# Kernel optimization log

Hardware: AMD Instinct MI355X
Metric: run time of the kernel (lower is better)

Reference implementation:

```python
import jax, jax.numpy as jnp
import numpy as np

N_HEAD, D_HEAD, D_MODEL = 16, 64, 1024
BSZ, QLEN, MEMLEN = 4, 1024, 1024
KLEN = QLEN + MEMLEN
LN_EPS = 1e-5


def _rel_shift(x):
    # x: [b, q, k, n] -> Transformer-XL relative shift
    b, q, k, n = x.shape
    x = jnp.pad(x, ((0, 0), (0, 0), (1, 0), (0, 0)))  # [b, q, k+1, n]
    x = x.reshape(b, k + 1, q, n)[:, 1:]
    return x.reshape(b, q, k, n)


def _layer_norm(x, gamma, beta):
    mu = jnp.mean(x, axis=-1, keepdims=True)
    var = jnp.var(x, axis=-1, keepdims=True)
    return (x - mu) * jax.lax.rsqrt(var + LN_EPS) * gamma + beta


def setup_inputs() -> dict:
    key = jax.random.key(0)
    ks = jax.random.split(key, 8)
    w = jax.random.normal(ks[0], (BSZ, QLEN, D_MODEL), dtype=jnp.float32)
    r = jax.random.normal(ks[1], (1, KLEN, D_MODEL), dtype=jnp.float32)
    mem = jax.random.normal(ks[2], (BSZ, MEMLEN, D_MODEL), dtype=jnp.float32)
    # causal mask: key j visible iff j <= i + MEMLEN; 1 = masked
    i = jnp.arange(QLEN)[:, None]
    j = jnp.arange(KLEN)[None, :]
    attention_mask = (j > i + MEMLEN).astype(jnp.int32)
    s = 0.02
    qkv_w = jax.random.normal(ks[3], (3 * N_HEAD * D_HEAD, D_MODEL), dtype=jnp.float32) * s
    r_w = jax.random.normal(ks[4], (N_HEAD * D_HEAD, D_MODEL), dtype=jnp.float32) * s
    o_w = jax.random.normal(ks[5], (D_MODEL, N_HEAD * D_HEAD), dtype=jnp.float32) * s
    r_r_bias = jax.random.normal(ks[6], (N_HEAD, D_HEAD), dtype=jnp.float32) * s
    r_w_bias = jax.random.normal(ks[7], (N_HEAD, D_HEAD), dtype=jnp.float32) * s
    ln_gamma = jnp.ones((D_MODEL,), dtype=jnp.float32)
    ln_beta = jnp.zeros((D_MODEL,), dtype=jnp.float32)
    return {"w": w, "r": r, "mem": mem, "attention_mask": attention_mask,
            "qkv_w": qkv_w, "r_w": r_w, "o_w": o_w,
            "r_r_bias": r_r_bias, "r_w_bias": r_w_bias,
            "ln_gamma": ln_gamma, "ln_beta": ln_beta}


def reference(w, r, mem, attention_mask, qkv_w, r_w, o_w, r_r_bias, r_w_bias, ln_gamma, ln_beta):
    bsz, qlen, d_model = w.shape
    n_head, d_head = r_r_bias.shape
    scale = 1.0 / (d_head ** 0.5)
    cat = jnp.concatenate([mem, w], axis=1)                 # [b, klen, dm]
    heads = cat @ qkv_w.T                                   # post-lnorm: no pre-LN
    q, k, v = jnp.split(heads, 3, axis=-1)
    q = q[:, -qlen:]
    klen = k.shape[1]
    q = q.reshape(bsz, qlen, n_head, d_head)
    k = k.reshape(bsz, klen, n_head, d_head)
    v = v.reshape(bsz, klen, n_head, d_head)
    rk = (r @ r_w.T).reshape(-1, n_head, d_head)            # [rlen, n, d]
    AC = jnp.einsum('bind,bjnd->bijn', q + r_w_bias, k)
    BD = _rel_shift(jnp.einsum('bind,jnd->bijn', q + r_r_bias, rk))
    score = (AC + BD) * scale                               # [b, q, k, n]
    mask = (attention_mask == 1)[None, :, :, None]
    score = jnp.where(mask, -1e30, score)
    prob = jax.nn.softmax(score, axis=2)                    # softmax over keys
    vec = jnp.einsum('bijn,bjnd->bind', prob, v).reshape(bsz, qlen, n_head * d_head)
    attn_out = vec @ o_w.T
    # post layer-norm, deepnorm_alpha defaults to 1.0, dropout is identity (eval)
    return _layer_norm(w + attn_out, ln_gamma, ln_beta)
```

## Files before the change

### kernel.cpp

```cpp
#include <hip/hip_runtime.h>

typedef __attribute__((ext_vector_type(8))) __bf16 bf16x8;
typedef __attribute__((ext_vector_type(4))) __bf16 bf16x4;
typedef __attribute__((ext_vector_type(4))) float f32x4;

#define SCALE_LOG2E 0.18033688011112042f

__device__ __forceinline__ f32x4 mfma16(bf16x8 a, bf16x8 b, f32x4 c) {
  return __builtin_amdgcn_mfma_f32_16x16x32_bf16(a, b, c, 0, 0, 0);
}

__device__ __forceinline__ void gload_lds16(const void* g, void* l) {
  __builtin_amdgcn_global_load_lds(
      (__attribute__((address_space(1))) void*)(void*)g,
      (__attribute__((address_space(3))) void*)l, 16, 0, 0);
}

__device__ __forceinline__ bf16x8 ldsfrag(const __bf16* base, int row, int lc) {
  return *(const bf16x8*)(base + row * 64 + ((lc ^ (row & 7)) << 3));
}


__global__ __launch_bounds__(256) void cast_plain(const float* __restrict__ in,
                                                  __bf16* __restrict__ out) {
  size_t t = (size_t)blockIdx.x * 256 + threadIdx.x;
  const float4* p = (const float4*)(in + t * 8);
  float4 a = p[0], b = p[1];
  bf16x8 v;
  v[0] = (__bf16)a.x; v[1] = (__bf16)a.y; v[2] = (__bf16)a.z; v[3] = (__bf16)a.w;
  v[4] = (__bf16)b.x; v[5] = (__bf16)b.y; v[6] = (__bf16)b.z; v[7] = (__bf16)b.w;
  *(bf16x8*)(out + t * 8) = v;
}

__global__ __launch_bounds__(256) void cast_cat(const float* __restrict__ mem,
                                                const float* __restrict__ w,
                                                __bf16* __restrict__ out) {
  size_t t = (size_t)blockIdx.x * 256 + threadIdx.x;
  size_t o = t * 8;
  int c = (int)(o & 1023);
  int row = (int)(o >> 10);
  int tt = row & 2047;
  int b = row >> 11;
  const float* src = (tt < 1024)
      ? (mem + ((size_t)(b * 1024 + tt) * 1024 + c))
      : (w + ((size_t)(b * 1024 + (tt - 1024)) * 1024 + c));
  float4 a = ((const float4*)src)[0], d = ((const float4*)src)[1];
  bf16x8 v;
  v[0] = (__bf16)a.x; v[1] = (__bf16)a.y; v[2] = (__bf16)a.z; v[3] = (__bf16)a.w;
  v[4] = (__bf16)d.x; v[5] = (__bf16)d.y; v[6] = (__bf16)d.z; v[7] = (__bf16)d.w;
  *(bf16x8*)(out + o) = v;
}

template <int MODE>
__global__ __launch_bounds__(256, 2) void gemm_bt(const __bf16* __restrict__ A,
                                                  const __bf16* __restrict__ B,
                                                  __bf16* __restrict__ Cb,
                                                  float* __restrict__ Cf,
                                                  const float* __restrict__ Res,
                                                  int M, int N, int K, int skipq) {
  if (skipq && blockIdx.x < 8 && (blockIdx.y & 15) < 8) return;
  __shared__ __bf16 As[128 * 32];
  __shared__ __bf16 Bs[128 * 32];
  const int tid = threadIdx.x;
  const int wid = tid >> 6, lane = tid & 63;
  const int l15 = lane & 15, lhi = lane >> 4;
  const int wr = wid >> 1, wc = wid & 1;
  const size_t arow0 = (size_t)blockIdx.y * 128;
  const size_t brow0 = (size_t)blockIdx.x * 128;

  f32x4 acc[4][4] = {};

  const int c0 = tid, c1 = tid + 256;
  const int r0 = c0 >> 2, o0 = (c0 & 3) * 8;
  const int r1 = c1 >> 2, o1 = (c1 & 3) * 8;
  const __bf16* ga0 = A + (arow0 + r0) * K + o0;
  const __bf16* ga1 = A + (arow0 + r1) * K + o1;
  const __bf16* gb0 = B + (brow0 + r0) * K + o0;
  const __bf16* gb1 = B + (brow0 + r1) * K + o1;
  __bf16* la0 = As + wid * 512;
  __bf16* la1 = As + 2048 + wid * 512;
  __bf16* lb0 = Bs + wid * 512;
  __bf16* lb1 = Bs + 2048 + wid * 512;

  for (int k0 = 0; k0 < K; k0 += 32) {
    gload_lds16(ga0 + k0, la0);
    gload_lds16(ga1 + k0, la1);
    gload_lds16(gb0 + k0, lb0);
    gload_lds16(gb1 + k0, lb1);
    __syncthreads();
    bf16x8 af[4], bf[4];
#pragma unroll
    for (int m = 0; m < 4; ++m)
      af[m] = *(const bf16x8*)(As + (wr * 64 + m * 16 + l15) * 32 + lhi * 8);
#pragma unroll
    for (int n = 0; n < 4; ++n)
      bf[n] = *(const bf16x8*)(Bs + (wc * 64 + n * 16 + l15) * 32 + lhi * 8);
#pragma unroll
    for (int m = 0; m < 4; ++m)
#pragma unroll
      for (int n = 0; n < 4; ++n)
        acc[m][n] = mfma16(af[m], bf[n], acc[m][n]);
    __syncthreads();
  }

#pragma unroll
  for (int m = 0; m < 4; ++m)
#pragma unroll
    for (int n = 0; n < 4; ++n) {
      size_t row = arow0 + wr * 64 + m * 16 + lhi * 4;
      size_t col = brow0 + wc * 64 + n * 16 + l15;
#pragma unroll
      for (int j = 0; j < 4; ++j) {
        size_t idx = (row + j) * (size_t)N + col;
        float v = acc[m][n][j];
        if (MODE == 0) Cb[idx] = (__bf16)v;
        else Cf[idx] = v + Res[idx];
      }
    }
}

__global__ __launch_bounds__(256) void vtrans_kernel(const __bf16* __restrict__ heads,
                                                     __bf16* __restrict__ vT) {
  __shared__ __bf16 T[64][66];
  const int j0 = blockIdx.x * 64;
  const int h = blockIdx.y, b = blockIdx.z;
  const int tid = threadIdx.x;
  {
    int jj = tid >> 2, dq = tid & 3;
    const __bf16* src = heads + ((size_t)(b * 2048 + j0 + jj)) * 3072 + 2048 + h * 64 + dq * 16;
    bf16x8 a = *(const bf16x8*)src;
    bf16x8 c = *(const bf16x8*)(src + 8);
#pragma unroll
    for (int e = 0; e < 8; ++e) { T[jj][dq * 16 + e] = a[e]; T[jj][dq * 16 + 8 + e] = c[e]; }
  }
  __syncthreads();
  {
    int d = tid >> 2, jq = tid & 3;
    bf16x8 o0, o1;
#pragma unroll
    for (int e = 0; e < 8; ++e) { o0[e] = T[jq * 16 + e][d]; o1[e] = T[jq * 16 + 8 + e][d]; }
    __bf16* dst = vT + ((size_t)((b * 16 + h) * 64 + d)) * 2048 + j0 + jq * 16;
    *(bf16x8*)dst = o0;
    *(bf16x8*)(dst + 8) = o1;
  }
}

__global__ __launch_bounds__(256) void ackb_kernel(const __bf16* __restrict__ heads,
                                                   const float* __restrict__ r_w_bias,
                                                   float* __restrict__ ackb) {
  int gid = blockIdx.x * 256 + threadIdx.x;
  int j = gid & 2047, bh = gid >> 11, b = bh >> 4, h = bh & 15;
  const __bf16* kp = heads + ((size_t)(b * 2048 + j)) * 3072 + 1024 + h * 64;
  const float* bw = r_w_bias + h * 64;
  float s = 0.f;
#pragma unroll
  for (int o = 0; o < 8; ++o) {
    bf16x8 kv = *(const bf16x8*)(kp + o * 8);
#pragma unroll
    for (int e = 0; e < 8; ++e) s += (float)kv[e] * bw[o * 8 + e];
  }
  ackb[(size_t)bh * 2048 + j] = s * SCALE_LOG2E;
}

__global__ __launch_bounds__(256) void brk_kernel(const __bf16* __restrict__ rk,
                                                  const float* __restrict__ r_r_bias,
                                                  float* __restrict__ brk) {
  int gid = blockIdx.x * 256 + threadIdx.x;
  int t = gid % 2304, h = gid / 2304;
  float s = 0.f;
  if (t < 2048) {
    const __bf16* rp = rk + (size_t)t * 1024 + h * 64;
    const float* br = r_r_bias + h * 64;
#pragma unroll
    for (int o = 0; o < 8; ++o) {
      bf16x8 rv = *(const bf16x8*)(rp + o * 8);
#pragma unroll
      for (int e = 0; e < 8; ++e) s += (float)rv[e] * br[o * 8 + e];
    }
  }
  brk[(size_t)h * 2304 + t] = s * SCALE_LOG2E;
}

__global__ __launch_bounds__(256) void attn_kernel(
    const __bf16* __restrict__ heads, const __bf16* __restrict__ rk,
    const __bf16* __restrict__ vT, const float* __restrict__ ackb,
    const float* __restrict__ brk, __bf16* __restrict__ vec) {
  __shared__ __bf16 Ks[2 * 4096];
  __shared__ __bf16 Vt[2 * 4096];
  __shared__ __bf16 Pool[4][2112];

  const int lin = blockIdx.x;
  const int seq = lin >> 3;
  const int bq = 15 - (seq >> 3);
  const int rem = seq & 7;
  const int b = rem >> 1;
  const int h = (lin & 7) + ((rem & 1) << 3);
  const int base = bq << 6;

  const int tid = threadIdx.x;
  const int wid = tid >> 6, lane = tid & 63;
  const int l15 = lane & 15, lhi = lane >> 4;
  const int i0 = base + wid * 16;

  const int srow8 = lane >> 3;
  const int sch = (lane & 7) ^ (srow8 & 7);

  bf16x8 q0, q1;
  {
    const __bf16* qp =
        heads + ((size_t)(b * 2048 + 1024 + i0 + l15)) * 3072 + h * 64 + lhi * 8;
    bf16x8 a = *(const bf16x8*)qp;
    bf16x8 c = *(const bf16x8*)(qp + 32);
#pragma unroll
    for (int e = 0; e < 8; ++e) {
      q0[e] = (__bf16)((float)a[e] * SCALE_LOG2E);
      q1[e] = (__bf16)((float)c[e] * SCALE_LOG2E);
    }
  }

  const float* ackbp = ackb + ((size_t)(b * 16 + h)) * 2048;
  const float* brkp = brk + (size_t)h * 2304;
  __bf16* BPW = Pool[wid];

  float m_run = -1e30f, l_run = 0.f;
  f32x4 accv[4] = {};

#define STAGE_KV(J0, BUF)                                                              \
  do {                                                                                 \
    const __bf16* kst = heads +                                                        \
        ((size_t)(b * 2048 + (J0) + wid * 16 + srow8)) * 3072 + 1024 + h * 64 + sch * 8; \
    gload_lds16(kst, Ks + (BUF) * 4096 + wid * 16 * 64);                               \
    gload_lds16(kst + (size_t)8 * 3072, Ks + (BUF) * 4096 + (wid * 16 + 8) * 64);      \
    const __bf16* vst = vT +                                                           \
        ((size_t)((b * 16 + h) * 64 + wid * 16 + srow8)) * 2048 + (J0) + sch * 8;      \
    gload_lds16(vst, Vt + (BUF) * 4096 + wid * 16 * 64);                               \
    gload_lds16(vst + (size_t)8 * 2048, Vt + (BUF) * 4096 + (wid * 16 + 8) * 64);      \
  } while (0)

  bf16x8 rka[5][2];
  STAGE_KV(0, 0);
  {
    const int tb0 = 1008 - i0;
#pragma unroll
    for (int ct = 0; ct < 5; ++ct) {
      int t = min(tb0 + ct * 16 + l15, 2047);
      const __bf16* rp = rk + (size_t)t * 1024 + h * 64 + lhi * 8;
      rka[ct][0] = *(const bf16x8*)rp;
      rka[ct][1] = *(const bf16x8*)(rp + 32);
    }
  }

  const int jmaxb = min(2048, base + 1088);
  for (int j0 = 0; j0 < jmaxb; j0 += 64) {
    const int buf = (j0 >> 6) & 1;
    __syncthreads();
    if (j0 + 64 < jmaxb) STAGE_KV(j0 + 64, buf ^ 1);
    if (j0 >= i0 + 1040) continue;

    const __bf16* KsC = Ks + buf * 4096;
    const __bf16* VtC = Vt + buf * 4096;
    const int tbase = j0 + 1008 - i0;

#pragma unroll
    for (int ct = 0; ct < 5; ++ct) {
      int cb = ct * 16 + lhi * 4;
      f32x4 init = *(const f32x4*)(brkp + tbase + cb);
      f32x4 bd = mfma16(rka[ct][1], q1, mfma16(rka[ct][0], q0, init));
      bf16x4 bv;
      bv[0] = (__bf16)bd[0]; bv[1] = (__bf16)bd[1];
      bv[2] = (__bf16)bd[2]; bv[3] = (__bf16)bd[3];
      *(bf16x4*)(BPW + l15 * 132 + cb) = bv;
    }
    rka[0][0] = rka[4][0];
    rka[0][1] = rka[4][1];
#pragma unroll
    for (int ct = 1; ct < 5; ++ct) {
      int t = min(tbase + 64 + ct * 16 + l15, 2047);
      const __bf16* rp = rk + (size_t)t * 1024 + h * 64 + lhi * 8;
      rka[ct][0] = *(const bf16x8*)rp;
      rka[ct][1] = *(const bf16x8*)(rp + 32);
    }

    f32x4 st[4];
#pragma unroll
    for (int jt = 0; jt < 4; ++jt) {
      bf16x8 k0 = ldsfrag(KsC, jt * 16 + l15, lhi);
      bf16x8 k1 = ldsfrag(KsC, jt * 16 + l15, 4 + lhi);
      f32x4 init = *(const f32x4*)(ackbp + j0 + jt * 16 + lhi * 4);
      st[jt] = mfma16(k1, q1, mfma16(k0, q0, init));
    }

    float sv[4][4];
#pragma unroll
    for (int jt = 0; jt < 4; ++jt)
#pragma unroll
      for (int r2 = 0; r2 < 4; ++r2) {
        int jl = jt * 16 + lhi * 4 + r2;
        sv[jt][r2] = st[jt][r2] + (float)BPW[l15 * 132 + jl + 15 - l15];
      }
    if (j0 + 63 > i0 + 1024) {
#pragma unroll
      for (int jt = 0; jt < 4; ++jt)
#pragma unroll
        for (int r2 = 0; r2 < 4; ++r2) {
          int jl = jt * 16 + lhi * 4 + r2;
          if (j0 + jl > i0 + l15 + 1024) sv[jt][r2] = -1e30f;
        }
    }

    float mx = sv[0][0];
#pragma unroll
    for (int jt = 0; jt < 4; ++jt)
#pragma unroll
      for (int r2 = 0; r2 < 4; ++r2) mx = fmaxf(mx, sv[jt][r2]);
    mx = fmaxf(mx, __shfl_xor(mx, 16, 64));
    mx = fmaxf(mx, __shfl_xor(mx, 32, 64));
    const bool resc = __any(mx > m_run + 8.0f);
    const float mn = resc ? fmaxf(m_run, mx) : m_run;
    float rs = 0.f;
#pragma unroll
    for (int jt = 0; jt < 4; ++jt)
#pragma unroll
      for (int r2 = 0; r2 < 4; ++r2) {
        float p = exp2f(sv[jt][r2] - mn);
        sv[jt][r2] = p;
        rs += p;
      }
    rs += __shfl_xor(rs, 16, 64);
    rs += __shfl_xor(rs, 32, 64);
    if (resc) {
      float corr = exp2f(m_run - mn);
      float c4[4];
#pragma unroll
      for (int r2 = 0; r2 < 4; ++r2) c4[r2] = __shfl(corr, lhi * 4 + r2, 64);
#pragma unroll
      for (int dt = 0; dt < 4; ++dt)
#pragma unroll
        for (int r2 = 0; r2 < 4; ++r2) accv[dt][r2] *= c4[r2];
      m_run = mn;
      l_run = l_run * corr + rs;
    } else {
      l_run += rs;
    }

#pragma unroll
    for (int jt = 0; jt < 4; ++jt) {
      bf16x4 pv;
      pv[0] = (__bf16)sv[jt][0]; pv[1] = (__bf16)sv[jt][1];
      pv[2] = (__bf16)sv[jt][2]; pv[3] = (__bf16)sv[jt][3];
      *(bf16x4*)(BPW + l15 * 72 + jt * 16 + lhi * 4) = pv;
    }
    bf16x8 ap0 = *(const bf16x8*)(BPW + l15 * 72 + lhi * 8);
    bf16x8 ap1 = *(const bf16x8*)(BPW + l15 * 72 + 32 + lhi * 8);
#pragma unroll
    for (int dt = 0; dt < 4; ++dt) {
      bf16x8 vf0 = ldsfrag(VtC, dt * 16 + l15, lhi);
      bf16x8 vf1 = ldsfrag(VtC, dt * 16 + l15, 4 + lhi);
      accv[dt] = mfma16(ap1, vf1, mfma16(ap0, vf0, accv[dt]));
    }
  }
#undef STAGE_KV

  float inv4[4];
#pragma unroll
  for (int r2 = 0; r2 < 4; ++r2) inv4[r2] = 1.0f / __shfl(l_run, lhi * 4 + r2, 64);
#pragma unroll
  for (int dt = 0; dt < 4; ++dt)
#pragma unroll
    for (int r2 = 0; r2 < 4; ++r2) {
      int i = i0 + lhi * 4 + r2;
      float v = accv[dt][r2] * inv4[r2];
      vec[((size_t)(b * 1024 + i)) * 1024 + h * 64 + dt * 16 + l15] = (__bf16)v;
    }
}

__global__ __launch_bounds__(256) void ln_kernel(const float* __restrict__ pre,
                                                 const float* __restrict__ gamma,
                                                 const float* __restrict__ beta,
                                                 float* __restrict__ out) {
  const int row = blockIdx.x;
  const int tid = threadIdx.x;
  const float4 v = ((const float4*)(pre + (size_t)row * 1024))[tid];
  float s = v.x + v.y + v.z + v.w;
  float s2 = v.x * v.x + v.y * v.y + v.z * v.z + v.w * v.w;
#pragma unroll
  for (int off = 1; off < 64; off <<= 1) {
    s += __shfl_xor(s, off, 64);
    s2 += __shfl_xor(s2, off, 64);
  }
  __shared__ float red[8];
  const int wid = tid >> 6;
  if ((tid & 63) == 0) { red[wid * 2] = s; red[wid * 2 + 1] = s2; }
  __syncthreads();
  s = red[0] + red[2] + red[4] + red[6];
  s2 = red[1] + red[3] + red[5] + red[7];
  float mu = s * (1.0f / 1024.0f);
  float var = s2 * (1.0f / 1024.0f) - mu * mu;
  float rstd = rsqrtf(var + 1e-5f);
  float4 g = ((const float4*)gamma)[tid];
  float4 be = ((const float4*)beta)[tid];
  float4 o;
  o.x = (v.x - mu) * rstd * g.x + be.x;
  o.y = (v.y - mu) * rstd * g.y + be.y;
  o.z = (v.z - mu) * rstd * g.z + be.z;
  o.w = (v.w - mu) * rstd * g.w + be.w;
  ((float4*)(out + (size_t)row * 1024))[tid] = o;
}

extern "C" void kernel_launch(void* const* d_in, const int* in_sizes, int n_in,
                              void* d_out, int out_size, void* d_ws, size_t ws_size,
                              hipStream_t stream) {
  const float* w = (const float*)d_in[0];
  const float* r = (const float*)d_in[1];
  const float* mem = (const float*)d_in[2];
  const float* qkv_w = (const float*)d_in[4];
  const float* r_w = (const float*)d_in[5];
  const float* o_w = (const float*)d_in[6];
  const float* r_r_bias = (const float*)d_in[7];
  const float* r_w_bias = (const float*)d_in[8];
  const float* gamma = (const float*)d_in[9];
  const float* beta = (const float*)d_in[10];
  float* out = (float*)d_out;

  char* ws = (char*)d_ws;
  const size_t MB = 1024 * 1024;
  __bf16* catB = (__bf16*)(ws + 0);
  __bf16* vT = (__bf16*)(ws + 0);
  float* pre = (float*)(ws + 0);
  __bf16* qkvwB = (__bf16*)(ws + 16 * MB);
  __bf16* rB = (__bf16*)(ws + 22 * MB);
  __bf16* rwB = (__bf16*)(ws + 26 * MB);
  __bf16* owB = (__bf16*)(ws + 28 * MB);
  __bf16* headsB = (__bf16*)(ws + 30 * MB);
  __bf16* rkB = (__bf16*)(ws + 78 * MB);
  __bf16* vecB = (__bf16*)(ws + 82 * MB);
  float* ackbF = (float*)(ws + 90 * MB);
  float* brkF = (float*)(ws + 91 * MB);

  cast_cat<<<4096, 256, 0, stream>>>(mem, w, catB);
  cast_plain<<<1536, 256, 0, stream>>>(qkv_w, qkvwB);
  cast_plain<<<1024, 256, 0, stream>>>(r, rB);
  cast_plain<<<512, 256, 0, stream>>>(r_w, rwB);
  cast_plain<<<512, 256, 0, stream>>>(o_w, owB);

  gemm_bt<0><<<dim3(24, 64), 256, 0, stream>>>(catB, qkvwB, headsB, nullptr, nullptr,
                                               8192, 3072, 1024, 1);
  gemm_bt<0><<<dim3(8, 16), 256, 0, stream>>>(rB, rwB, rkB, nullptr, nullptr,
                                              2048, 1024, 1024, 0);

  vtrans_kernel<<<dim3(32, 16, 4), 256, 0, stream>>>(headsB, vT);
  ackb_kernel<<<512, 256, 0, stream>>>(headsB, r_w_bias, ackbF);
  brk_kernel<<<144, 256, 0, stream>>>(rkB, r_r_bias, brkF);

  attn_kernel<<<1024, 256, 0, stream>>>(headsB, rkB, vT, ackbF, brkF, vecB);

  gemm_bt<1><<<dim3(8, 32), 256, 0, stream>>>(vecB, owB, nullptr, pre, w,
                                              4096, 1024, 1024, 0);
  ln_kernel<<<4096, 256, 0, stream>>>(pre, gamma, beta, out);
}
```

Measured before the change: 354.4 us.

## Restructure attention kernel to 32x32 MFMA tiles with LDS-staged rk and 128-row blocks

The attention kernel now gives each wave 32 query rows instead of 16 and uses 32x32x16 bf16 MFMA in place of 16x16x32. Position-key (rk) rows are staged into LDS once per block instead of being loaded per wave from global memory. V fragments are read straight from global into registers, and K is single-buffered behind two barriers per tile instead of double-buffered. It also remaps blocks across XCDs for locality, adds setprio around the MFMA sections, uses packed bf16 converts, and halves the grid to 512 blocks, trading fewer concurrent blocks and the lost K/V prefetch overlap for more reuse per block.

```diff
diff --git a/kernel.cpp b/kernel.cpp
--- a/kernel.cpp
+++ b/kernel.cpp
@@ -3,11 +3,15 @@
 typedef __attribute__((ext_vector_type(8))) __bf16 bf16x8;
 typedef __attribute__((ext_vector_type(4))) __bf16 bf16x4;
 typedef __attribute__((ext_vector_type(4))) float f32x4;
+typedef __attribute__((ext_vector_type(16))) float f32x16;
 
 #define SCALE_LOG2E 0.18033688011112042f
 
 __device__ __forceinline__ f32x4 mfma16(bf16x8 a, bf16x8 b, f32x4 c) {
   return __builtin_amdgcn_mfma_f32_16x16x32_bf16(a, b, c, 0, 0, 0);
+}
+__device__ __forceinline__ f32x16 mfma32(bf16x8 a, bf16x8 b, f32x16 c) {
+  return __builtin_amdgcn_mfma_f32_32x32x16_bf16(a, b, c, 0, 0, 0);
 }
 
 __device__ __forceinline__ void gload_lds16(const void* g, void* l) {
@@ -181,196 +185,216 @@
   brk[(size_t)h * 2304 + t] = s * SCALE_LOG2E;
 }
 
-__global__ __launch_bounds__(256) void attn_kernel(
+__global__ __launch_bounds__(256, 2) void attn_kernel(
     const __bf16* __restrict__ heads, const __bf16* __restrict__ rk,
     const __bf16* __restrict__ vT, const float* __restrict__ ackb,
     const float* __restrict__ brk, __bf16* __restrict__ vec) {
-  __shared__ __bf16 Ks[2 * 4096];
-  __shared__ __bf16 Vt[2 * 4096];
-  __shared__ __bf16 Pool[4][2112];
+  __shared__ __bf16 Ks[64 * 64];
+  __shared__ __bf16 Rst[192 * 64];
+  __shared__ __bf16 BP[4][3200];
 
   const int lin = blockIdx.x;
-  const int seq = lin >> 3;
-  const int bq = 15 - (seq >> 3);
-  const int rem = seq & 7;
-  const int b = rem >> 1;
-  const int h = (lin & 7) + ((rem & 1) << 3);
-  const int base = bq << 6;
+  const int xcd = lin & 7, s = lin >> 3;
+  const int half = s >> 5, r5 = s & 31;
+  const int bh = xcd * 8 + (r5 >> 3) + half * 4;
+  const int bqr = r5 & 7;
+  const int bq = half ? bqr : 7 - bqr;
+  const int b = bh >> 4, h = bh & 15;
+  const int base = bq << 7;
 
   const int tid = threadIdx.x;
   const int wid = tid >> 6, lane = tid & 63;
-  const int l15 = lane & 15, lhi = lane >> 4;
-  const int i0 = base + wid * 16;
+  const int il = lane & 31, hi5 = lane >> 5;
+  const int i0 = base + wid * 32;
 
   const int srow8 = lane >> 3;
   const int sch = (lane & 7) ^ (srow8 & 7);
 
-  bf16x8 q0, q1;
+  bf16x8 qf[4];
   {
     const __bf16* qp =
-        heads + ((size_t)(b * 2048 + 1024 + i0 + l15)) * 3072 + h * 64 + lhi * 8;
-    bf16x8 a = *(const bf16x8*)qp;
-    bf16x8 c = *(const bf16x8*)(qp + 32);
-#pragma unroll
-    for (int e = 0; e < 8; ++e) {
-      q0[e] = (__bf16)((float)a[e] * SCALE_LOG2E);
-      q1[e] = (__bf16)((float)c[e] * SCALE_LOG2E);
-    }
-  }
-
-  const float* ackbp = ackb + ((size_t)(b * 16 + h)) * 2048;
+        heads + ((size_t)(b * 2048 + 1024 + i0 + il)) * 3072 + h * 64 + hi5 * 8;
+#pragma unroll
+    for (int ks = 0; ks < 4; ++ks) {
+      bf16x8 a = *(const bf16x8*)(qp + ks * 16);
+      bf16x8 o;
+#pragma unroll
+      for (int e = 0; e < 8; ++e) o[e] = (__bf16)((float)a[e] * SCALE_LOG2E);
+      qf[ks] = o;
+    }
+  }
+
+  const float* ackbp = ackb + (size_t)bh * 2048;
   const float* brkp = brk + (size_t)h * 2304;
-  __bf16* BPW = Pool[wid];
+  const __bf16* vTp = vT + (size_t)bh * 64 * 2048;
+  __bf16* Bw = BP[wid];
 
   float m_run = -1e30f, l_run = 0.f;
-  f32x4 accv[4] = {};
-
-#define STAGE_KV(J0, BUF)                                                              \
-  do {                                                                                 \
-    const __bf16* kst = heads +                                                        \
-        ((size_t)(b * 2048 + (J0) + wid * 16 + srow8)) * 3072 + 1024 + h * 64 + sch * 8; \
-    gload_lds16(kst, Ks + (BUF) * 4096 + wid * 16 * 64);                               \
-    gload_lds16(kst + (size_t)8 * 3072, Ks + (BUF) * 4096 + (wid * 16 + 8) * 64);      \
-    const __bf16* vst = vT +                                                           \
-        ((size_t)((b * 16 + h) * 64 + wid * 16 + srow8)) * 2048 + (J0) + sch * 8;      \
-    gload_lds16(vst, Vt + (BUF) * 4096 + wid * 16 * 64);                               \
-    gload_lds16(vst + (size_t)8 * 2048, Vt + (BUF) * 4096 + (wid * 16 + 8) * 64);      \
-  } while (0)
-
-  bf16x8 rka[5][2];
-  STAGE_KV(0, 0);
-  {
-    const int tb0 = 1008 - i0;
-#pragma unroll
-    for (int ct = 0; ct < 5; ++ct) {
-      int t = min(tb0 + ct * 16 + l15, 2047);
-      const __bf16* rp = rk + (size_t)t * 1024 + h * 64 + lhi * 8;
-      rka[ct][0] = *(const bf16x8*)rp;
-      rka[ct][1] = *(const bf16x8*)(rp + 32);
-    }
-  }
-
-  const int jmaxb = min(2048, base + 1088);
+  f32x16 accv[2] = {};
+
+  const int rkoff = 96 - wid * 32;
+  const int jmaxb = min(2048, base + 1152);
   for (int j0 = 0; j0 < jmaxb; j0 += 64) {
-    const int buf = (j0 >> 6) & 1;
     __syncthreads();
-    if (j0 + 64 < jmaxb) STAGE_KV(j0 + 64, buf ^ 1);
-    if (j0 >= i0 + 1040) continue;
-
-    const __bf16* KsC = Ks + buf * 4096;
-    const __bf16* VtC = Vt + buf * 4096;
-    const int tbase = j0 + 1008 - i0;
-
-#pragma unroll
-    for (int ct = 0; ct < 5; ++ct) {
-      int cb = ct * 16 + lhi * 4;
-      f32x4 init = *(const f32x4*)(brkp + tbase + cb);
-      f32x4 bd = mfma16(rka[ct][1], q1, mfma16(rka[ct][0], q0, init));
-      bf16x4 bv;
-      bv[0] = (__bf16)bd[0]; bv[1] = (__bf16)bd[1];
-      bv[2] = (__bf16)bd[2]; bv[3] = (__bf16)bd[3];
-      *(bf16x4*)(BPW + l15 * 132 + cb) = bv;
-    }
-    rka[0][0] = rka[4][0];
-    rka[0][1] = rka[4][1];
-#pragma unroll
-    for (int ct = 1; ct < 5; ++ct) {
-      int t = min(tbase + 64 + ct * 16 + l15, 2047);
-      const __bf16* rp = rk + (size_t)t * 1024 + h * 64 + lhi * 8;
-      rka[ct][0] = *(const bf16x8*)rp;
-      rka[ct][1] = *(const bf16x8*)(rp + 32);
-    }
-
-    f32x4 st[4];
-#pragma unroll
-    for (int jt = 0; jt < 4; ++jt) {
-      bf16x8 k0 = ldsfrag(KsC, jt * 16 + l15, lhi);
-      bf16x8 k1 = ldsfrag(KsC, jt * 16 + l15, 4 + lhi);
-      f32x4 init = *(const f32x4*)(ackbp + j0 + jt * 16 + lhi * 4);
-      st[jt] = mfma16(k1, q1, mfma16(k0, q0, init));
-    }
-
-    float sv[4][4];
-#pragma unroll
-    for (int jt = 0; jt < 4; ++jt)
-#pragma unroll
-      for (int r2 = 0; r2 < 4; ++r2) {
-        int jl = jt * 16 + lhi * 4 + r2;
-        sv[jt][r2] = st[jt][r2] + (float)BPW[l15 * 132 + jl + 15 - l15];
+    {
+      const __bf16* kst = heads +
+          ((size_t)(b * 2048 + j0 + wid * 16 + srow8)) * 3072 + 1024 + h * 64 + sch * 8;
+      gload_lds16(kst, Ks + (wid * 16) * 64);
+      gload_lds16(kst + (size_t)8 * 3072, Ks + (wid * 16 + 8) * 64);
+      const int rstart = j0 + 896 - base;
+#pragma unroll
+      for (int g = 0; g < 6; ++g) {
+        int dr = wid * 48 + g * 8;
+        int rg = min(rstart + dr + srow8, 2047);
+        gload_lds16(rk + ((size_t)rg << 10) + h * 64 + sch * 8, Rst + dr * 64);
+      }
+    }
+    __syncthreads();
+    if (j0 >= i0 + 1056) continue;
+
+    const int tbase = j0 + 992 - i0;
+
+    bf16x8 vfr[4][2];
+#pragma unroll
+    for (int jc = 0; jc < 4; ++jc)
+#pragma unroll
+      for (int dt = 0; dt < 2; ++dt)
+        vfr[jc][dt] = *(const bf16x8*)(vTp + (size_t)(dt * 32 + il) * 2048 +
+                                       j0 + jc * 16 + hi5 * 8);
+
+    __builtin_amdgcn_s_setprio(1);
+#pragma unroll
+    for (int ct = 0; ct < 3; ++ct) {
+      f32x16 ci;
+#pragma unroll
+      for (int qd = 0; qd < 4; ++qd) {
+        f32x4 b4 = *(const f32x4*)(brkp + tbase + ct * 32 + qd * 8 + hi5 * 4);
+#pragma unroll
+        for (int e = 0; e < 4; ++e) ci[qd * 4 + e] = b4[e];
+      }
+      const int ar = rkoff + ct * 32 + il;
+#pragma unroll
+      for (int ks = 0; ks < 4; ++ks)
+        ci = mfma32(ldsfrag(Rst, ar, ks * 2 + hi5), qf[ks], ci);
+#pragma unroll
+      for (int qd = 0; qd < 4; ++qd) {
+        union { unsigned u[2]; bf16x4 v; } pw;
+        asm("v_cvt_pk_bf16_f32 %0, %1, %2"
+            : "=v"(pw.u[0]) : "v"(ci[qd * 4 + 0]), "v"(ci[qd * 4 + 1]));
+        asm("v_cvt_pk_bf16_f32 %0, %1, %2"
+            : "=v"(pw.u[1]) : "v"(ci[qd * 4 + 2]), "v"(ci[qd * 4 + 3]));
+        *(bf16x4*)(Bw + il * 100 + ct * 32 + qd * 8 + hi5 * 4) = pw.v;
+      }
+    }
+
+    f32x16 st[2];
+#pragma unroll
+    for (int jt = 0; jt < 2; ++jt) {
+      f32x16 ci;
+#pragma unroll
+      for (int qd = 0; qd < 4; ++qd) {
+        f32x4 a4 = *(const f32x4*)(ackbp + j0 + jt * 32 + qd * 8 + hi5 * 4);
+#pragma unroll
+        for (int e = 0; e < 4; ++e) ci[qd * 4 + e] = a4[e];
+      }
+#pragma unroll
+      for (int ks = 0; ks < 4; ++ks)
+        ci = mfma32(ldsfrag(Ks, jt * 32 + il, ks * 2 + hi5), qf[ks], ci);
+      st[jt] = ci;
+    }
+    __builtin_amdgcn_s_setprio(0);
+
+    float sv[2][16];
+#pragma unroll
+    for (int jt = 0; jt < 2; ++jt)
+#pragma unroll
+      for (int rg = 0; rg < 16; ++rg) {
+        const int crow = (rg & 3) + 8 * (rg >> 2) + 4 * hi5;
+        const int c = jt * 32 + crow + 31 - il;
+        sv[jt][rg] = st[jt][rg] + (float)Bw[il * 100 + c];
       }
     if (j0 + 63 > i0 + 1024) {
 #pragma unroll
-      for (int jt = 0; jt < 4; ++jt)
-#pragma unroll
-        for (int r2 = 0; r2 < 4; ++r2) {
-          int jl = jt * 16 + lhi * 4 + r2;
-          if (j0 + jl > i0 + l15 + 1024) sv[jt][r2] = -1e30f;
+      for (int jt = 0; jt < 2; ++jt)
+#pragma unroll
+        for (int rg = 0; rg < 16; ++rg) {
+          const int crow = (rg & 3) + 8 * (rg >> 2) + 4 * hi5;
+          if (j0 + jt * 32 + crow > i0 + il + 1024) sv[jt][rg] = -1e30f;
         }
     }
 
     float mx = sv[0][0];
 #pragma unroll
-    for (int jt = 0; jt < 4; ++jt)
-#pragma unroll
-      for (int r2 = 0; r2 < 4; ++r2) mx = fmaxf(mx, sv[jt][r2]);
-    mx = fmaxf(mx, __shfl_xor(mx, 16, 64));
+    for (int jt = 0; jt < 2; ++jt)
+#pragma unroll
+      for (int rg = 0; rg < 16; ++rg) mx = fmaxf(mx, sv[jt][rg]);
     mx = fmaxf(mx, __shfl_xor(mx, 32, 64));
     const bool resc = __any(mx > m_run + 8.0f);
     const float mn = resc ? fmaxf(m_run, mx) : m_run;
     float rs = 0.f;
 #pragma unroll
-    for (int jt = 0; jt < 4; ++jt)
-#pragma unroll
-      for (int r2 = 0; r2 < 4; ++r2) {
-        float p = exp2f(sv[jt][r2] - mn);
-        sv[jt][r2] = p;
+    for (int jt = 0; jt < 2; ++jt)
+#pragma unroll
+      for (int rg = 0; rg < 16; ++rg) {
+        float p = exp2f(sv[jt][rg] - mn);
+        sv[jt][rg] = p;
         rs += p;
       }
-    rs += __shfl_xor(rs, 16, 64);
     rs += __shfl_xor(rs, 32, 64);
     if (resc) {
-      float corr = exp2f(m_run - mn);
-      float c4[4];
-#pragma unroll
-      for (int r2 = 0; r2 < 4; ++r2) c4[r2] = __shfl(corr, lhi * 4 + r2, 64);
-#pragma unroll
-      for (int dt = 0; dt < 4; ++dt)
-#pragma unroll
-        for (int r2 = 0; r2 < 4; ++r2) accv[dt][r2] *= c4[r2];
+      const float corr = exp2f(m_run - mn);
       m_run = mn;
       l_run = l_run * corr + rs;
+      float c16[16];
+#pragma unroll
+      for (int rg = 0; rg < 16; ++rg) {
+        const int crow = (rg & 3) + 8 * (rg >> 2) + 4 * hi5;
+        c16[rg] = __shfl(corr, crow, 64);
+      }
+#pragma unroll
+      for (int dt = 0; dt < 2; ++dt)
+#pragma unroll
+        for (int rg = 0; rg < 16; ++rg) accv[dt][rg] *= c16[rg];
     } else {
       l_run += rs;
     }
 
 #pragma unroll
-    for (int jt = 0; jt < 4; ++jt) {
-      bf16x4 pv;
-      pv[0] = (__bf16)sv[jt][0]; pv[1] = (__bf16)sv[jt][1];
-      pv[2] = (__bf16)sv[jt][2]; pv[3] = (__bf16)sv[jt][3];
-      *(bf16x4*)(BPW + l15 * 72 + jt * 16 + lhi * 4) = pv;
-    }
-    bf16x8 ap0 = *(const bf16x8*)(BPW + l15 * 72 + lhi * 8);
-    bf16x8 ap1 = *(const bf16x8*)(BPW + l15 * 72 + 32 + lhi * 8);
-#pragma unroll
-    for (int dt = 0; dt < 4; ++dt) {
-      bf16x8 vf0 = ldsfrag(VtC, dt * 16 + l15, lhi);
-      bf16x8 vf1 = ldsfrag(VtC, dt * 16 + l15, 4 + lhi);
-      accv[dt] = mfma16(ap1, vf1, mfma16(ap0, vf0, accv[dt]));
-    }
-  }
-#undef STAGE_KV
-
-  float inv4[4];
-#pragma unroll
-  for (int r2 = 0; r2 < 4; ++r2) inv4[r2] = 1.0f / __shfl(l_run, lhi * 4 + r2, 64);
-#pragma unroll
-  for (int dt = 0; dt < 4; ++dt)
-#pragma unroll
-    for (int r2 = 0; r2 < 4; ++r2) {
-      int i = i0 + lhi * 4 + r2;
-      float v = accv[dt][r2] * inv4[r2];
-      vec[((size_t)(b * 1024 + i)) * 1024 + h * 64 + dt * 16 + l15] = (__bf16)v;
+    for (int jt = 0; jt < 2; ++jt)
+#pragma unroll
+      for (int qd = 0; qd < 4; ++qd) {
+        union { unsigned u[2]; bf16x4 v; } pw;
+        asm("v_cvt_pk_bf16_f32 %0, %1, %2"
+            : "=v"(pw.u[0]) : "v"(sv[jt][qd * 4 + 0]), "v"(sv[jt][qd * 4 + 1]));
+        asm("v_cvt_pk_bf16_f32 %0, %1, %2"
+            : "=v"(pw.u[1]) : "v"(sv[jt][qd * 4 + 2]), "v"(sv[jt][qd * 4 + 3]));
+        *(bf16x4*)(Bw + il * 88 + jt * 32 + qd * 8 + hi5 * 4) = pw.v;
+      }
+
+    __builtin_amdgcn_s_setprio(1);
+#pragma unroll
+    for (int jc = 0; jc < 4; ++jc) {
+      bf16x8 ap = *(const bf16x8*)(Bw + il * 88 + jc * 16 + hi5 * 8);
+#pragma unroll
+      for (int dt = 0; dt < 2; ++dt)
+        accv[dt] = mfma32(ap, vfr[jc][dt], accv[dt]);
+    }
+    __builtin_amdgcn_s_setprio(0);
+  }
+
+  float linv[16];
+#pragma unroll
+  for (int rg = 0; rg < 16; ++rg) {
+    const int crow = (rg & 3) + 8 * (rg >> 2) + 4 * hi5;
+    linv[rg] = 1.0f / __shfl(l_run, crow, 64);
+  }
+#pragma unroll
+  for (int dt = 0; dt < 2; ++dt)
+#pragma unroll
+    for (int rg = 0; rg < 16; ++rg) {
+      const int crow = (rg & 3) + 8 * (rg >> 2) + 4 * hi5;
+      vec[((size_t)(b * 1024 + i0 + crow)) * 1024 + h * 64 + dt * 32 + il] =
+          (__bf16)(accv[dt][rg] * linv[rg]);
     }
 }
 
@@ -452,7 +476,7 @@
   ackb_kernel<<<512, 256, 0, stream>>>(headsB, r_w_bias, ackbF);
   brk_kernel<<<144, 256, 0, stream>>>(rkB, r_r_bias, brkF);
 
-  attn_kernel<<<1024, 256, 0, stream>>>(headsB, rkB, vT, ackbF, brkF, vecB);
+  attn_kernel<<<512, 256, 0, stream>>>(headsB, rkB, vT, ackbF, brkF, vecB);
 
   gemm_bt<1><<<dim3(8, 32), 256, 0, stream>>>(vecB, owB, nullptr, pre, w,
                                               4096, 1024, 1024, 0);
```

Result: faster. 316.4 us (-10.7%).
